# Kernel tuning notes

Hardware: AMD Instinct MI355X
Metric: run time of the kernel (lower is better)

The kernel has to match this reference:

```python
import jax, jax.numpy as jnp
import numpy as np

EMBED_DIM = 1024
NUM_HEADS = 16
HEAD_DIM = EMBED_DIM // NUM_HEADS
BATCH = 2
SEQ = 2048


def setup_inputs() -> dict:
    key = jax.random.key(0)
    ks = jax.random.split(key, 10)
    s = 1.0 / np.sqrt(EMBED_DIM)
    inp = {
        "query": jax.random.normal(ks[0], (BATCH, SEQ, EMBED_DIM), jnp.float32),
        # Linear weights stored as [in, out] (y = x @ W + b)
        "wq": jax.random.normal(ks[1], (EMBED_DIM, EMBED_DIM), jnp.float32) * s,
        "bq": jnp.zeros((EMBED_DIM,), jnp.float32),
        "wk": jax.random.normal(ks[2], (EMBED_DIM, EMBED_DIM), jnp.float32) * s,
        "bk": jnp.zeros((EMBED_DIM,), jnp.float32),
        "wv": jax.random.normal(ks[3], (EMBED_DIM, EMBED_DIM), jnp.float32) * s,
        "bv": jnp.zeros((EMBED_DIM,), jnp.float32),
        "wo": jax.random.normal(ks[4], (EMBED_DIM, EMBED_DIM), jnp.float32) * s,
        "bo": jnp.zeros((EMBED_DIM,), jnp.float32),
        "temperature": jnp.float32(HEAD_DIM),  # learnable temperature, init = head_dim
    }
    return inp


def reference(query, wq, bq, wk, bk, wv, bv, wo, bo, temperature):
    B, S, E = query.shape
    # self-attention: key = value = query
    Q = (query @ wq + bq).reshape(B, S, NUM_HEADS, HEAD_DIM).transpose(0, 2, 1, 3)
    K = (query @ wk + bk).reshape(B, S, NUM_HEADS, HEAD_DIM).transpose(0, 2, 1, 3)
    V = (query @ wv + bv).reshape(B, S, NUM_HEADS, HEAD_DIM).transpose(0, 2, 1, 3)
    # squared Euclidean distances: ||q||^2 + ||k||^2 - 2<q,k>
    q_sq = jnp.sum(Q * Q, axis=-1, keepdims=True)          # (B,H,Sq,1)
    k_sq = jnp.sum(K * K, axis=-1, keepdims=True)          # (B,H,Sk,1)
    qk = jnp.einsum("bhqd,bhkd->bhqk", Q, K)
    d_sq = jnp.maximum(q_sq + jnp.swapaxes(k_sq, -2, -1) - 2.0 * qk, 0.0)
    attn = jax.nn.softmax(-d_sq / temperature, axis=-1)    # (B,H,Sq,Sk)
    out = jnp.einsum("bhqk,bhkd->bhqd", attn, V)
    out = out.transpose(0, 2, 1, 3).reshape(B, S, E)
    return out @ wo + bo
```

## Files before the change

### kernel.cpp

```cpp
#include <hip/hip_runtime.h>
#include <stdint.h>
#include <stddef.h>


#define LOG2E 1.44269504088896f

typedef __attribute__((ext_vector_type(8))) short bf16x8;
typedef __attribute__((ext_vector_type(4))) float f32x4;
typedef __attribute__((ext_vector_type(4))) unsigned short u16x4;

__device__ __forceinline__ unsigned short f2b(float f) {
  union { float f; unsigned int u; } x; x.f = f;
  unsigned int u = x.u;
  u += 0x7fffu + ((u >> 16) & 1u);
  return (unsigned short)(u >> 16);
}
__device__ __forceinline__ float b2f(unsigned short s) {
  union { unsigned int u; float f; } x; x.u = ((unsigned int)s) << 16;
  return x.f;
}
__device__ __forceinline__ unsigned int fbits(float f) {
  union { float f; unsigned int u; } x; x.f = f; return x.u;
}

#define GLD_LDS(g, l) __builtin_amdgcn_global_load_lds( \
    (const __attribute__((address_space(1))) void*)(g), \
    (__attribute__((address_space(3))) void*)(l), 16, 0, 0)

__global__ void prep_kernel(const float* __restrict__ X,
                            const float* __restrict__ wq, const float* __restrict__ wk,
                            const float* __restrict__ wv, const float* __restrict__ wo,
                            unsigned short* __restrict__ Xb,
                            unsigned short* __restrict__ WTqkv, unsigned short* __restrict__ WTo) {
  int z = blockIdx.z;
  if (z == 4) {
    size_t base = ((size_t)(blockIdx.y * 16 + blockIdx.x)) * 16384;
    #pragma unroll
    for (int j = 0; j < 16; ++j) {
      size_t i = base + (size_t)(j * 256 + threadIdx.x) * 4;
      f32x4 v = *(const f32x4*)&X[i];
      u16x4 o;
      #pragma unroll
      for (int k = 0; k < 4; ++k) o[k] = f2b(v[k]);
      *(u16x4*)&Xb[i] = o;
    }
    return;
  }
  __shared__ float tile[64][65];
  const float* src = (z == 0) ? wq : (z == 1) ? wk : (z == 2) ? wv : wo;
  unsigned short* dst = (z < 3) ? (WTqkv + (size_t)z * 1024 * 1024) : WTo;
  int k0 = blockIdx.y * 64, n0 = blockIdx.x * 64;
  int rr = threadIdx.x >> 6, cc = threadIdx.x & 63;
  #pragma unroll
  for (int p = 0; p < 16; ++p) {
    int row = p * 4 + rr;
    tile[row][cc] = src[(size_t)(k0 + row) * 1024 + n0 + cc];
  }
  __syncthreads();
  #pragma unroll
  for (int p = 0; p < 16; ++p) {
    int row = p * 4 + rr;
    dst[(size_t)(n0 + row) * 1024 + k0 + cc] = f2b(tile[cc][row]);
  }
}

__global__ __launch_bounds__(256, 3) void gemm_qkv_kernel(
    const unsigned short* __restrict__ X, const unsigned short* __restrict__ WT,
    const float* __restrict__ bq, const float* __restrict__ bk, const float* __restrict__ bv,
    const float* __restrict__ temp,
    unsigned short* __restrict__ Qb, unsigned short* __restrict__ Kb,
    unsigned short* __restrict__ VTo, float* __restrict__ ks2) {
  __shared__ __align__(16) unsigned short smem[16896];
  unsigned short* As = smem;
  unsigned short* Bs = smem + 8192;
  const int t = threadIdx.x, w = t >> 6, lane = t & 63;
  const int r = lane & 15, q4 = lane >> 4;
  const int m0 = blockIdx.y * 128, n0 = blockIdx.x * 128;
  const int wr = (w >> 1) * 64, wc = (w & 1) * 64;
  const unsigned short* Xg = X + (size_t)m0 * 1024;
  const unsigned short* Wg = WT + (size_t)n0 * 1024;
  f32x4 acc[4][4] = {};
  for (int k0 = 0; k0 < 1024; k0 += 64) {
    #pragma unroll
    for (int g = 0; g < 4; ++g) {
      int slot = g * 256 + t;
      int kh = slot >> 9, row = (slot >> 2) & 127, ko = (slot & 3) * 8;
      GLD_LDS(Xg + (size_t)row * 1024 + k0 + kh * 32 + ko, &As[(g * 256 + w * 64) * 8]);
      GLD_LDS(Wg + (size_t)row * 1024 + k0 + kh * 32 + ko, &Bs[(g * 256 + w * 64) * 8]);
    }
    __syncthreads();
    #pragma unroll
    for (int kh = 0; kh < 2; ++kh) {
      bf16x8 af[4], bfr[4];
      #pragma unroll
      for (int mf = 0; mf < 4; ++mf)
        af[mf] = *(const bf16x8*)&As[kh * 4096 + (wr + mf * 16 + r) * 32 + q4 * 8];
      #pragma unroll
      for (int nf = 0; nf < 4; ++nf)
        bfr[nf] = *(const bf16x8*)&Bs[kh * 4096 + (wc + nf * 16 + r) * 32 + q4 * 8];
      #pragma unroll
      for (int mf = 0; mf < 4; ++mf)
        #pragma unroll
        for (int nf = 0; nf < 4; ++nf)
          acc[mf][nf] = __builtin_amdgcn_mfma_f32_16x16x32_bf16(af[mf], bfr[nf], acc[mf][nf], 0, 0, 0);
    }
    __syncthreads();
  }
  const int nblk = n0 >> 10;
  if (nblk == 0) {
    const int nc0 = n0 & 1023;
    #pragma unroll
    for (int nf = 0; nf < 4; ++nf) {
      int n = nc0 + wc + nf * 16 + r;
      float bb = bq[n];
      #pragma unroll
      for (int mf = 0; mf < 4; ++mf) {
        int m = m0 + wr + mf * 16 + q4 * 4;
        f32x4 v = acc[mf][nf];
        #pragma unroll
        for (int i = 0; i < 4; ++i)
          Qb[(size_t)(m + i) * 1024 + n] = f2b(v[i] + bb);
      }
    }
  } else if (nblk == 1) {
    const float sc = LOG2E / temp[0];
    const int nc0 = n0 & 1023;
    float s2a[4][4] = {};
    #pragma unroll
    for (int nf = 0; nf < 4; ++nf) {
      int n = nc0 + wc + nf * 16 + r;
      float bb = bk[n];
      #pragma unroll
      for (int mf = 0; mf < 4; ++mf) {
        int m = m0 + wr + mf * 16 + q4 * 4;
        f32x4 v = acc[mf][nf];
        #pragma unroll
        for (int i = 0; i < 4; ++i) {
          unsigned short os = f2b(v[i] + bb);
          Kb[(size_t)(m + i) * 1024 + n] = os;
          float xb = b2f(os);
          s2a[mf][i] += xb * xb;
        }
      }
    }
    #pragma unroll
    for (int mf = 0; mf < 4; ++mf)
      #pragma unroll
      for (int i = 0; i < 4; ++i) {
        float v = s2a[mf][i];
        v += __shfl_xor(v, 1, 64);
        v += __shfl_xor(v, 2, 64);
        v += __shfl_xor(v, 4, 64);
        v += __shfl_xor(v, 8, 64);
        s2a[mf][i] = v * sc;
      }
    if (r == 0) {
      int hh = (nc0 + wc) >> 6;
      #pragma unroll
      for (int mf = 0; mf < 4; ++mf) {
        int m = m0 + wr + mf * 16 + q4 * 4;
        int bb2 = m >> 11, ss = m & 2047;
        #pragma unroll
        for (int i = 0; i < 4; ++i)
          ks2[(size_t)(bb2 * 16 + hh) * 2048 + ss + i] = s2a[mf][i];
      }
    }
  } else {
    unsigned short* Vt = smem;
    const int c0 = n0 - 2048;
    const int head = w & 1;
    #pragma unroll
    for (int nf = 0; nf < 4; ++nf) {
      int c = c0 + wc + nf * 16 + r;
      float bb = bv[c];
      int d = c & 63;
      #pragma unroll
      for (int mf = 0; mf < 4; ++mf) {
        int mloc = wr + mf * 16 + q4 * 4;
        int G = mloc >> 6;
        int k6 = mloc & 63;
        int pos = (k6 >> 5) * 32 + ((k6 & 15) >> 2) * 8 + ((k6 >> 4) & 1) * 4;
        f32x4 v = acc[mf][nf];
        u16x4 pk;
        #pragma unroll
        for (int i = 0; i < 4; ++i) pk[i] = f2b(v[i] + bb);
        *(u16x4*)&Vt[(head * 64 + d) * 132 + G * 64 + pos] = pk;
      }
    }
    __syncthreads();
    int row = t >> 1, ch = t & 1;
    int hd = row >> 6, dd = row & 63;
    int hglob = (c0 >> 6) + hd;
    int bb2 = m0 >> 11, s0 = m0 & 2047;
    unsigned short* dst = &VTo[((size_t)((bb2 * 16 + hglob) * 64 + dd)) * 2048 + s0 + ch * 64];
    const unsigned short* srcL = &Vt[(hd * 64 + dd) * 132 + ch * 64];
    #pragma unroll
    for (int k2 = 0; k2 < 16; ++k2)
      *(u16x4*)&dst[k2 * 4] = *(const u16x4*)&srcL[k2 * 4];
  }
}

__global__ __launch_bounds__(256, 4) void flash_kernel(
    const unsigned short* __restrict__ Qb, const unsigned short* __restrict__ Kb,
    const unsigned short* __restrict__ VT, const float* __restrict__ ks2,
    const float* __restrict__ temp, unsigned short* __restrict__ AO) {
  __shared__ __align__(16) unsigned short Ks[2][64 * 64];
  __shared__ __align__(16) unsigned short Vs[2][64 * 64];
  const int t = threadIdx.x, w = t >> 6, lane = t & 63;
  const int r = lane & 15, q4 = lane >> 4;
  const int bh = blockIdx.y, b = bh >> 4, h = bh & 15;
  const int q0 = blockIdx.x * 64;
  const float cc = 2.0f * LOG2E / temp[0];

  bf16x8 qf[2];
  {
    int sq = q0 + w * 16 + r;
    const unsigned short* qp = Qb + (size_t)(b * 2048 + sq) * 1024 + h * 64;
    #pragma unroll
    for (int ks = 0; ks < 2; ++ks) qf[ks] = *(const bf16x8*)(qp + ks * 32 + q4 * 8);
  }

  f32x4 accO[4] = {};
  f32x4 lsum = {};
  bf16x8 ones;
  #pragma unroll
  for (int j = 0; j < 8; ++j) ones[j] = (short)0x3F80;

  const unsigned short* Kg = Kb + ((size_t)b * 2048) * 1024 + h * 64;
  const unsigned short* Vg = VT + ((size_t)bh * 64) * 2048;
  const float* kqb = ks2 + bh * 2048;

  const unsigned short* kp0 = Kg + (size_t)(t >> 2) * 1024 + (t & 3) * 8;
  const unsigned short* kp1 = kp0 + 32;
  int dd0 = t >> 3;
  const unsigned short* vp0 = Vg + (size_t)dd0 * 2048 + ((t & 7) ^ (dd0 & 7)) * 8;
  const unsigned short* vp1 = vp0 + (size_t)32 * 2048;
  GLD_LDS(kp0, &Ks[0][t * 8]);
  GLD_LDS(kp1, &Ks[0][(256 + t) * 8]);
  GLD_LDS(vp0, &Vs[0][t * 8]);
  GLD_LDS(vp1, &Vs[0][(256 + t) * 8]);
  kp0 += 65536; kp1 += 65536; vp0 += 64; vp1 += 64;

  #pragma unroll 2
  for (int c = 0; c < 32; ++c) {
    const int buf = c & 1;
    __syncthreads();
    if (c < 31) {
      GLD_LDS(kp0, &Ks[buf ^ 1][t * 8]);
      GLD_LDS(kp1, &Ks[buf ^ 1][(256 + t) * 8]);
      GLD_LDS(vp0, &Vs[buf ^ 1][t * 8]);
      GLD_LDS(vp1, &Vs[buf ^ 1][(256 + t) * 8]);
      kp0 += 65536; kp1 += 65536; vp0 += 64; vp1 += 64;
    }
    f32x4 kq[4];
    #pragma unroll
    for (int kfm = 0; kfm < 4; ++kfm)
      kq[kfm] = *(const f32x4*)&kqb[c * 64 + kfm * 16 + q4 * 4];

    f32x4 accST[4] = {};
    #pragma unroll
    for (int ks = 0; ks < 2; ++ks) {
      #pragma unroll
      for (int kfm = 0; kfm < 4; ++kfm) {
        bf16x8 ka = *(const bf16x8*)&Ks[buf][(ks * 64 + kfm * 16 + r) * 32 + q4 * 8];
        accST[kfm] = __builtin_amdgcn_mfma_f32_16x16x32_bf16(ka, qf[ks], accST[kfm], 0, 0, 0);
      }
    }

    bf16x8 pf[2];
    #pragma unroll
    for (int cb = 0; cb < 2; ++cb) {
      unsigned int dw[4];
      #pragma unroll
      for (int half = 0; half < 2; ++half) {
        int kfm = cb * 2 + half;
        float pp[4];
        #pragma unroll
        for (int i = 0; i < 4; ++i) {
          float u = __builtin_fmaf(cc, accST[kfm][i], -kq[kfm][i]);
          pp[i] = __builtin_amdgcn_exp2f(u);
        }
        dw[half * 2 + 0] = (fbits(pp[0]) >> 16) | (fbits(pp[1]) & 0xFFFF0000u);
        dw[half * 2 + 1] = (fbits(pp[2]) >> 16) | (fbits(pp[3]) & 0xFFFF0000u);
      }
      union { unsigned int d[4]; bf16x8 v; } cv;
      cv.d[0] = dw[0]; cv.d[1] = dw[1]; cv.d[2] = dw[2]; cv.d[3] = dw[3];
      pf[cb] = cv.v;
    }

    #pragma unroll
    for (int cb = 0; cb < 2; ++cb) {
      lsum = __builtin_amdgcn_mfma_f32_16x16x32_bf16(pf[cb], ones, lsum, 0, 0, 0);
      #pragma unroll
      for (int df = 0; df < 4; ++df) {
        int dloc = df * 16 + r;
        int un = dloc * 8 + ((cb * 4 + q4) ^ (dloc & 7));
        bf16x8 vb = *(const bf16x8*)&Vs[buf][un * 8];
        accO[df] = __builtin_amdgcn_mfma_f32_16x16x32_bf16(pf[cb], vb, accO[df], 0, 0, 0);
      }
    }
  }
  {
    float inv[4];
    #pragma unroll
    for (int i = 0; i < 4; ++i) inv[i] = 1.0f / lsum[i];
    #pragma unroll
    for (int df = 0; df < 4; ++df) {
      int d = df * 16 + r;
      #pragma unroll
      for (int i = 0; i < 4; ++i) {
        int sq = q0 + w * 16 + q4 * 4 + i;
        AO[(size_t)(b * 2048 + sq) * 1024 + h * 64 + d] = f2b(accO[df][i] * inv[i]);
      }
    }
  }
}

__global__ __launch_bounds__(256, 2) void gemm_out_kernel(
    const unsigned short* __restrict__ A, const unsigned short* __restrict__ WT,
    const float* __restrict__ bo, float* __restrict__ Out) {
  __shared__ __align__(16) unsigned short As[2 * 128 * 32];
  __shared__ __align__(16) unsigned short Bs[2 * 64 * 32];
  const int t = threadIdx.x, w = t >> 6, lane = t & 63;
  const int r = lane & 15, q4 = lane >> 4;
  const int m0 = blockIdx.y * 128, n0 = blockIdx.x * 64;
  const int wr = (w >> 1) * 64, wc = (w & 1) * 32;
  const unsigned short* Ag = A + (size_t)m0 * 1024;
  const unsigned short* Wg = WT + (size_t)n0 * 1024;
  f32x4 acc[4][2] = {};
  for (int k0 = 0; k0 < 1024; k0 += 64) {
    #pragma unroll
    for (int g = 0; g < 4; ++g) {
      int slot = g * 256 + t;
      int kh = slot >> 9, row = (slot >> 2) & 127, ko = (slot & 3) * 8;
      GLD_LDS(Ag + (size_t)row * 1024 + k0 + kh * 32 + ko, &As[(g * 256 + w * 64) * 8]);
    }
    #pragma unroll
    for (int g = 0; g < 2; ++g) {
      int slot = g * 256 + t;
      int kh = slot >> 8, row = (slot >> 2) & 63, ko = (slot & 3) * 8;
      GLD_LDS(Wg + (size_t)row * 1024 + k0 + kh * 32 + ko, &Bs[(g * 256 + w * 64) * 8]);
    }
    __syncthreads();
    #pragma unroll
    for (int kh = 0; kh < 2; ++kh) {
      bf16x8 af[4], bfr[2];
      #pragma unroll
      for (int mf = 0; mf < 4; ++mf)
        af[mf] = *(const bf16x8*)&As[kh * 4096 + (wr + mf * 16 + r) * 32 + q4 * 8];
      #pragma unroll
      for (int nf = 0; nf < 2; ++nf)
        bfr[nf] = *(const bf16x8*)&Bs[kh * 2048 + (wc + nf * 16 + r) * 32 + q4 * 8];
      #pragma unroll
      for (int mf = 0; mf < 4; ++mf)
        #pragma unroll
        for (int nf = 0; nf < 2; ++nf)
          acc[mf][nf] = __builtin_amdgcn_mfma_f32_16x16x32_bf16(af[mf], bfr[nf], acc[mf][nf], 0, 0, 0);
    }
    __syncthreads();
  }
  #pragma unroll
  for (int nf = 0; nf < 2; ++nf) {
    int n = n0 + wc + nf * 16 + r;
    float bb = bo[n];
    #pragma unroll
    for (int mf = 0; mf < 4; ++mf) {
      int m = m0 + wr + mf * 16 + q4 * 4;
      f32x4 v = acc[mf][nf];
      #pragma unroll
      for (int i = 0; i < 4; ++i)
        Out[(size_t)(m + i) * 1024 + n] = v[i] + bb;
    }
  }
}

extern "C" void kernel_launch(void* const* d_in, const int* in_sizes, int n_in,
                              void* d_out, int out_size, void* d_ws, size_t ws_size,
                              hipStream_t stream) {
  const float* X    = (const float*)d_in[0];
  const float* wq   = (const float*)d_in[1];
  const float* bq   = (const float*)d_in[2];
  const float* wk   = (const float*)d_in[3];
  const float* bk   = (const float*)d_in[4];
  const float* wv   = (const float*)d_in[5];
  const float* bv   = (const float*)d_in[6];
  const float* wo   = (const float*)d_in[7];
  const float* bo   = (const float*)d_in[8];
  const float* temp = (const float*)d_in[9];
  float* Out = (float*)d_out;

  char* ws = (char*)d_ws;
  unsigned short* Xb    = (unsigned short*)ws; ws += (size_t)4096 * 1024 * 2;
  unsigned short* WTqkv = (unsigned short*)ws; ws += (size_t)3072 * 1024 * 2;
  unsigned short* WTo   = (unsigned short*)ws; ws += (size_t)1024 * 1024 * 2;
  unsigned short* Qb    = (unsigned short*)ws; ws += (size_t)4096 * 1024 * 2;
  unsigned short* Kb    = (unsigned short*)ws; ws += (size_t)4096 * 1024 * 2;
  unsigned short* VT    = (unsigned short*)ws; ws += (size_t)4096 * 1024 * 2;
  float* ks2 = (float*)ws; ws += (size_t)65536 * 4;
  unsigned short* AO = Xb;

  prep_kernel<<<dim3(16, 16, 5), 256, 0, stream>>>(X, wq, wk, wv, wo, Xb, WTqkv, WTo);
  gemm_qkv_kernel<<<dim3(24, 32), 256, 0, stream>>>(Xb, WTqkv, bq, bk, bv, temp, Qb, Kb, VT, ks2);
  flash_kernel<<<dim3(32, 32), 256, 0, stream>>>(Qb, Kb, VT, ks2, temp, AO);
  gemm_out_kernel<<<dim3(16, 32), 256, 0, stream>>>(AO, WTo, bo, Out);
}
```

Measured before the change: 196.2 us.

## Process two query tiles per warp in flash kernel to reuse K/V fragments

Each flash block now handles 128 queries instead of 64: every warp owns two 16-row query groups and applies each K and V fragment loaded from LDS to both. The goal is to halve LDS reads and global K/V traffic per query and to raise MFMA density per load. In exchange, register use roughly doubles, so launch bounds drop to 2 blocks per CU, and the grid shrinks to 512 blocks. That lowers occupancy and the ability to hide latency.

```diff
diff --git a/kernel.cpp b/kernel.cpp
--- a/kernel.cpp
+++ b/kernel.cpp
@@ -200,7 +200,7 @@
   }
 }
 
-__global__ __launch_bounds__(256, 4) void flash_kernel(
+__global__ __launch_bounds__(256, 2) void flash_kernel(
     const unsigned short* __restrict__ Qb, const unsigned short* __restrict__ Kb,
     const unsigned short* __restrict__ VT, const float* __restrict__ ks2,
     const float* __restrict__ temp, unsigned short* __restrict__ AO) {
@@ -209,19 +209,20 @@
   const int t = threadIdx.x, w = t >> 6, lane = t & 63;
   const int r = lane & 15, q4 = lane >> 4;
   const int bh = blockIdx.y, b = bh >> 4, h = bh & 15;
-  const int q0 = blockIdx.x * 64;
+  const int q0 = blockIdx.x * 128;
   const float cc = 2.0f * LOG2E / temp[0];
 
-  bf16x8 qf[2];
-  {
-    int sq = q0 + w * 16 + r;
+  bf16x8 qf[2][2];
+  #pragma unroll
+  for (int qg = 0; qg < 2; ++qg) {
+    int sq = q0 + w * 32 + qg * 16 + r;
     const unsigned short* qp = Qb + (size_t)(b * 2048 + sq) * 1024 + h * 64;
     #pragma unroll
-    for (int ks = 0; ks < 2; ++ks) qf[ks] = *(const bf16x8*)(qp + ks * 32 + q4 * 8);
-  }
-
-  f32x4 accO[4] = {};
-  f32x4 lsum = {};
+    for (int ks = 0; ks < 2; ++ks) qf[qg][ks] = *(const bf16x8*)(qp + ks * 32 + q4 * 8);
+  }
+
+  f32x4 accO[2][4] = {};
+  f32x4 lsum[2] = {};
   bf16x8 ones;
   #pragma unroll
   for (int j = 0; j < 8; ++j) ones[j] = (short)0x3F80;
@@ -257,60 +258,67 @@
     for (int kfm = 0; kfm < 4; ++kfm)
       kq[kfm] = *(const f32x4*)&kqb[c * 64 + kfm * 16 + q4 * 4];
 
-    f32x4 accST[4] = {};
+    f32x4 accST[2][4] = {};
     #pragma unroll
     for (int ks = 0; ks < 2; ++ks) {
       #pragma unroll
       for (int kfm = 0; kfm < 4; ++kfm) {
         bf16x8 ka = *(const bf16x8*)&Ks[buf][(ks * 64 + kfm * 16 + r) * 32 + q4 * 8];
-        accST[kfm] = __builtin_amdgcn_mfma_f32_16x16x32_bf16(ka, qf[ks], accST[kfm], 0, 0, 0);
-      }
-    }
-
-    bf16x8 pf[2];
+        accST[0][kfm] = __builtin_amdgcn_mfma_f32_16x16x32_bf16(ka, qf[0][ks], accST[0][kfm], 0, 0, 0);
+        accST[1][kfm] = __builtin_amdgcn_mfma_f32_16x16x32_bf16(ka, qf[1][ks], accST[1][kfm], 0, 0, 0);
+      }
+    }
+
+    bf16x8 pf[2][2];
+    #pragma unroll
+    for (int qg = 0; qg < 2; ++qg) {
+      #pragma unroll
+      for (int cb = 0; cb < 2; ++cb) {
+        unsigned int dw[4];
+        #pragma unroll
+        for (int half = 0; half < 2; ++half) {
+          int kfm = cb * 2 + half;
+          float pp[4];
+          #pragma unroll
+          for (int i = 0; i < 4; ++i) {
+            float u = __builtin_fmaf(cc, accST[qg][kfm][i], -kq[kfm][i]);
+            pp[i] = __builtin_amdgcn_exp2f(u);
+          }
+          dw[half * 2 + 0] = (fbits(pp[0]) >> 16) | (fbits(pp[1]) & 0xFFFF0000u);
+          dw[half * 2 + 1] = (fbits(pp[2]) >> 16) | (fbits(pp[3]) & 0xFFFF0000u);
+        }
+        union { unsigned int d[4]; bf16x8 v; } cv;
+        cv.d[0] = dw[0]; cv.d[1] = dw[1]; cv.d[2] = dw[2]; cv.d[3] = dw[3];
+        pf[qg][cb] = cv.v;
+      }
+    }
+
     #pragma unroll
     for (int cb = 0; cb < 2; ++cb) {
-      unsigned int dw[4];
-      #pragma unroll
-      for (int half = 0; half < 2; ++half) {
-        int kfm = cb * 2 + half;
-        float pp[4];
-        #pragma unroll
-        for (int i = 0; i < 4; ++i) {
-          float u = __builtin_fmaf(cc, accST[kfm][i], -kq[kfm][i]);
-          pp[i] = __builtin_amdgcn_exp2f(u);
-        }
-        dw[half * 2 + 0] = (fbits(pp[0]) >> 16) | (fbits(pp[1]) & 0xFFFF0000u);
-        dw[half * 2 + 1] = (fbits(pp[2]) >> 16) | (fbits(pp[3]) & 0xFFFF0000u);
-      }
-      union { unsigned int d[4]; bf16x8 v; } cv;
-      cv.d[0] = dw[0]; cv.d[1] = dw[1]; cv.d[2] = dw[2]; cv.d[3] = dw[3];
-      pf[cb] = cv.v;
-    }
-
-    #pragma unroll
-    for (int cb = 0; cb < 2; ++cb) {
-      lsum = __builtin_amdgcn_mfma_f32_16x16x32_bf16(pf[cb], ones, lsum, 0, 0, 0);
+      lsum[0] = __builtin_amdgcn_mfma_f32_16x16x32_bf16(pf[0][cb], ones, lsum[0], 0, 0, 0);
+      lsum[1] = __builtin_amdgcn_mfma_f32_16x16x32_bf16(pf[1][cb], ones, lsum[1], 0, 0, 0);
       #pragma unroll
       for (int df = 0; df < 4; ++df) {
         int dloc = df * 16 + r;
         int un = dloc * 8 + ((cb * 4 + q4) ^ (dloc & 7));
         bf16x8 vb = *(const bf16x8*)&Vs[buf][un * 8];
-        accO[df] = __builtin_amdgcn_mfma_f32_16x16x32_bf16(pf[cb], vb, accO[df], 0, 0, 0);
-      }
-    }
-  }
-  {
+        accO[0][df] = __builtin_amdgcn_mfma_f32_16x16x32_bf16(pf[0][cb], vb, accO[0][df], 0, 0, 0);
+        accO[1][df] = __builtin_amdgcn_mfma_f32_16x16x32_bf16(pf[1][cb], vb, accO[1][df], 0, 0, 0);
+      }
+    }
+  }
+  #pragma unroll
+  for (int qg = 0; qg < 2; ++qg) {
     float inv[4];
     #pragma unroll
-    for (int i = 0; i < 4; ++i) inv[i] = 1.0f / lsum[i];
+    for (int i = 0; i < 4; ++i) inv[i] = 1.0f / lsum[qg][i];
     #pragma unroll
     for (int df = 0; df < 4; ++df) {
       int d = df * 16 + r;
       #pragma unroll
       for (int i = 0; i < 4; ++i) {
-        int sq = q0 + w * 16 + q4 * 4 + i;
-        AO[(size_t)(b * 2048 + sq) * 1024 + h * 64 + d] = f2b(accO[df][i] * inv[i]);
+        int sq = q0 + w * 32 + qg * 16 + q4 * 4 + i;
+        AO[(size_t)(b * 2048 + sq) * 1024 + h * 64 + d] = f2b(accO[qg][df][i] * inv[i]);
       }
     }
   }
@@ -401,6 +409,6 @@
 
   prep_kernel<<<dim3(16, 16, 5), 256, 0, stream>>>(X, wq, wk, wv, wo, Xb, WTqkv, WTo);
   gemm_qkv_kernel<<<dim3(24, 32), 256, 0, stream>>>(Xb, WTqkv, bq, bk, bv, temp, Qb, Kb, VT, ks2);
-  flash_kernel<<<dim3(32, 32), 256, 0, stream>>>(Qb, Kb, VT, ks2, temp, AO);
+  flash_kernel<<<dim3(16, 32), 256, 0, stream>>>(Qb, Kb, VT, ks2, temp, AO);
   gemm_out_kernel<<<dim3(16, 32), 256, 0, stream>>>(AO, WTo, bo, Out);
 }
```

Result: slower. 202.6 us (+3.3%).
